# Optimization experiments

Measured on AMD Instinct MI355X. Metric: run time of the kernel, lower is better.

Reference implementation:

```python
import jax, jax.numpy as jnp
import numpy as np

N, K, D = 50000, 32, 128


def setup_inputs() -> dict:
    key = jax.random.key(0)
    k1, k2, k3, k4 = jax.random.split(key, 4)
    v_fea = jax.random.normal(k1, (N, D), dtype=jnp.float32)
    t_emb = jax.random.normal(k2, (N, D), dtype=jnp.float32)
    ef = jax.random.randint(k3, (N, K), 0, N, dtype=jnp.int64)
    # nn.Linear(2D, 2D, bias=False) weight, scaled like torch default init
    W = jax.random.normal(k4, (2 * D, 2 * D), dtype=jnp.float32) * (1.0 / np.sqrt(2 * D))
    return {"v_fea": v_fea, "t_emb": t_emb, "ef": ef, "W": W}


def reference(v_fea, t_emb, ef, W):
    # v: gathered neighbor features [N, K, D]
    v = v_fea[ef]
    # q: [N, 2D]; torch Linear applies x @ W.T
    q = jnp.concatenate([v_fea, t_emb], axis=-1)
    wq = q @ W.T                                   # [N, 2D]
    # k: [N, K, 2D]
    k = jnp.concatenate([v, t_emb[ef]], axis=-1)
    # per-edge score: bmm(k, wq[..., None]) -> [N, K]
    r = jnp.einsum("nkd,nd->nk", k, wq)
    r = jax.nn.softmax(r, axis=1)                  # softmax over neighbors
    # weighted sum over neighbors -> [N, D]
    ef_fea = jnp.einsum("nk,nkd->nd", r, v)
    return ef_fea
```

## Files before the change

kernel.cpp:

```cpp
#include <hip/hip_runtime.h>
#include <hip/hip_bf16.h>

#define D     128
#define TWO_D 256
#define KNB   32

typedef __attribute__((ext_vector_type(8))) short    s8;
typedef __attribute__((ext_vector_type(8))) _Float16 h8;
typedef __attribute__((ext_vector_type(2))) _Float16 h2v;
typedef __attribute__((ext_vector_type(4))) float    f4;

__device__ inline unsigned short f2h(float f) {
    return __builtin_bit_cast(unsigned short, (_Float16)f);
}
__device__ inline float h2f(unsigned short u) {
    return (float)__builtin_bit_cast(_Float16, u);
}

union v16u { s8 s; h2v h[4]; };

__device__ inline float dot8(s8 x, s8 w, float acc) {
#if __has_builtin(__builtin_amdgcn_fdot2)
    v16u ux, uw; ux.s = x; uw.s = w;
#pragma unroll
    for (int j = 0; j < 4; ++j)
        acc = __builtin_amdgcn_fdot2(ux.h[j], uw.h[j], acc, false);
#else
#pragma unroll
    for (int j = 0; j < 8; ++j)
        acc = fmaf(h2f((unsigned short)x[j]), h2f((unsigned short)w[j]), acc);
#endif
    return acc;
}

__global__ __launch_bounds__(256) void cast_kernel(
    const float* __restrict__ a, const float* __restrict__ b,
    unsigned short* __restrict__ oa, unsigned short* __restrict__ ob, int n4)
{
    int i = blockIdx.x * 256 + threadIdx.x;
    if (i >= n4) return;
    float4 x = ((const float4*)a)[i];
    float4 y = ((const float4*)b)[i];
    ushort4 px = make_ushort4(f2h(x.x), f2h(x.y), f2h(x.z), f2h(x.w));
    ushort4 py = make_ushort4(f2h(y.x), f2h(y.y), f2h(y.z), f2h(y.w));
    ((ushort4*)oa)[i] = px;
    ((ushort4*)ob)[i] = py;
}

#define BM 128
#define BN 128
#define BK 32
#define LDT 56

__global__ __launch_bounds__(256) void gemm_wq_mfma(
    const unsigned short* __restrict__ vh, const unsigned short* __restrict__ th,
    const float* __restrict__ W, unsigned short* __restrict__ wq_h, int M)
{
    __shared__ unsigned short As[BM][LDT];
    __shared__ unsigned short Bs[BN][LDT];

    const int tid  = threadIdx.x;
    const int w    = tid >> 6;
    const int lane = tid & 63;
    const int quad = lane >> 4;
    const int l16  = lane & 15;
    const int row0 = blockIdx.x * BM;
    const int i0   = blockIdx.y * BN;

    f4 acc[2][8] = {};

    const int srow = tid >> 1;
    const int seg  = tid & 1;
    int ga = row0 + srow; if (ga >= M) ga = M - 1;

    for (int kt = 0; kt < TWO_D; kt += BK) {
        const unsigned short* srcA = (kt < D) ? vh : th;
        const int kb = kt & (D - 1);
        const unsigned short* pa = srcA + (size_t)ga * D + kb + seg * 16;
        s8 a0 = *(const s8*)(pa);
        s8 a1 = *(const s8*)(pa + 8);
        const float* pb = W + (size_t)(i0 + srow) * TWO_D + kt + seg * 16;
        float4 b0 = *(const float4*)(pb);
        float4 b1 = *(const float4*)(pb + 4);
        float4 b2 = *(const float4*)(pb + 8);
        float4 b3 = *(const float4*)(pb + 12);

        __syncthreads();
        *(s8*)&As[srow][seg * 16]     = a0;
        *(s8*)&As[srow][seg * 16 + 8] = a1;
        {
            s8 q0, q1;
            q0[0]=(short)f2h(b0.x); q0[1]=(short)f2h(b0.y); q0[2]=(short)f2h(b0.z); q0[3]=(short)f2h(b0.w);
            q0[4]=(short)f2h(b1.x); q0[5]=(short)f2h(b1.y); q0[6]=(short)f2h(b1.z); q0[7]=(short)f2h(b1.w);
            q1[0]=(short)f2h(b2.x); q1[1]=(short)f2h(b2.y); q1[2]=(short)f2h(b2.z); q1[3]=(short)f2h(b2.w);
            q1[4]=(short)f2h(b3.x); q1[5]=(short)f2h(b3.y); q1[6]=(short)f2h(b3.z); q1[7]=(short)f2h(b3.w);
            *(s8*)&Bs[srow][seg * 16]     = q0;
            *(s8*)&Bs[srow][seg * 16 + 8] = q1;
        }
        __syncthreads();

        s8 af0 = *(const s8*)&As[w * 32 + l16][quad * 8];
        s8 af1 = *(const s8*)&As[w * 32 + 16 + l16][quad * 8];
#pragma unroll
        for (int nt = 0; nt < 8; ++nt) {
            s8 bf = *(const s8*)&Bs[nt * 16 + l16][quad * 8];
            acc[0][nt] = __builtin_amdgcn_mfma_f32_16x16x32_f16(
                __builtin_bit_cast(h8, af0), __builtin_bit_cast(h8, bf), acc[0][nt], 0, 0, 0);
            acc[1][nt] = __builtin_amdgcn_mfma_f32_16x16x32_f16(
                __builtin_bit_cast(h8, af1), __builtin_bit_cast(h8, bf), acc[1][nt], 0, 0, 0);
        }
    }

#pragma unroll
    for (int mt = 0; mt < 2; ++mt) {
#pragma unroll
        for (int nt = 0; nt < 8; ++nt) {
#pragma unroll
            for (int r = 0; r < 4; ++r) {
                int grow = row0 + w * 32 + mt * 16 + quad * 4 + r;
                if (grow < M)
                    wq_h[(size_t)grow * TWO_D + i0 + nt * 16 + l16] = f2h(acc[mt][nt][r]);
            }
        }
    }
}

__global__ __launch_bounds__(256) void attn_kernel(
    const unsigned short* __restrict__ vh, const unsigned short* __restrict__ th,
    const int* __restrict__ ef, const unsigned short* __restrict__ wq_h,
    float* __restrict__ outp, int M)
{
    __shared__ unsigned short v_cache[4][KNB][D];

    const int lane = threadIdx.x & 63;
    const int w    = threadIdx.x >> 6;
    const int n    = blockIdx.x * 4 + w;
    if (n >= M) return;

    const int l16  = lane & 15;
    const int gsel = (lane >> 4) & 1;
    const unsigned short* gsrc = (lane < 32) ? vh : th;

    s8 wq8 = *(const s8*)(wq_h + (size_t)n * TWO_D + ((lane >> 5) << 7) + l16 * 8);

    int eidx = 0;
    if (lane < KNB) eidx = ef[n * KNB + lane];

    s8 xs[16];
#pragma unroll
    for (int kk = 0; kk < 16; ++kk) {
        int e = __shfl(eidx, 2 * kk + gsel, 64);
        xs[kk] = *(const s8*)(gsrc + (size_t)e * D + l16 * 8);
    }

    float myscore = -1e30f;
#pragma unroll
    for (int kk = 0; kk < 16; ++kk) {
        const int k = 2 * kk;
        if (lane < 32) *(s8*)&v_cache[w][k + gsel][l16 * 8] = xs[kk];
        float p = dot8(xs[kk], wq8, 0.f);
#pragma unroll
        for (int off = 8; off > 0; off >>= 1) p += __shfl_xor(p, off, 64);
        p += __shfl_xor(p, 32, 64);
        float po = __shfl_xor(p, 16, 64);
        float s_even = gsel ? po : p;
        float s_odd  = gsel ? p  : po;
        if (lane == k)     myscore = s_even;
        if (lane == k + 1) myscore = s_odd;
    }

    float mx = myscore;
#pragma unroll
    for (int off = 16; off > 0; off >>= 1) mx = fmaxf(mx, __shfl_xor(mx, off, 64));
    float ex  = __expf(myscore - mx);
    float sum = ex;
#pragma unroll
    for (int off = 16; off > 0; off >>= 1) sum += __shfl_xor(sum, off, 64);
    float r = ex / sum;

    float2 o = make_float2(0.f, 0.f);
#pragma unroll
    for (int k = 0; k < KNB; ++k) {
        float rk = __shfl(r, k, 64);
        unsigned int pq = *(const unsigned int*)&v_cache[w][k][lane * 2];
        o.x = fmaf(rk, h2f((unsigned short)(pq & 0xFFFFu)), o.x);
        o.y = fmaf(rk, h2f((unsigned short)(pq >> 16)), o.y);
    }
    *(float2*)(outp + (size_t)n * D + lane * 2) = o;
}

extern "C" void kernel_launch(void* const* d_in, const int* in_sizes, int n_in,
                              void* d_out, int out_size, void* d_ws, size_t ws_size,
                              hipStream_t stream)
{
    const float* v_fea = (const float*)d_in[0];
    const float* t_emb = (const float*)d_in[1];
    const int*   ef    = (const int*)d_in[2];
    const float* W     = (const float*)d_in[3];
    float* outp = (float*)d_out;

    const int M = in_sizes[0] / D;
    char* ws = (char*)d_ws;
    unsigned short* wq_h = (unsigned short*)ws;
    unsigned short* vh   = (unsigned short*)(ws + (size_t)M * TWO_D * 2);
    unsigned short* th   = (unsigned short*)(ws + (size_t)M * TWO_D * 2 + (size_t)M * D * 2);

    const int n4 = M * D / 4;
    cast_kernel<<<(n4 + 255) / 256, 256, 0, stream>>>(v_fea, t_emb, vh, th, n4);

    dim3 gg((M + BM - 1) / BM, TWO_D / BN);
    gemm_wq_mfma<<<gg, 256, 0, stream>>>(vh, th, W, wq_h, M);
    attn_kernel<<<(M + 3) / 4, 256, 0, stream>>>(vh, th, ef, wq_h, outp, M);
}
```

Before: 230.0 us.

## Interleave fp16 v/t rows and use single-pass online-softmax gather attention

The cast kernel now writes v_fea and t_emb into one interleaved fp16 buffer of shape [N, 2D]. Each gathered neighbour therefore becomes a single contiguous 512-byte row, and the GEMM reads its A operand from that one buffer. The attention kernel drops the LDS cache. Each 16-lane group handles one neighbour per step, and the kernel uses an online (running-max) softmax with register accumulation, software-prefetching the second half of the neighbour rows. This is meant to cut the scattered gather transactions, the LDS traffic and the separate softmax passes. The cost is extra lane shuffles, wasted accumulation on the t half of each row, and higher register pressure.

```diff
diff --git a/kernel.cpp b/kernel.cpp
--- a/kernel.cpp
+++ b/kernel.cpp
@@ -35,16 +35,22 @@
 
 __global__ __launch_bounds__(256) void cast_kernel(
     const float* __restrict__ a, const float* __restrict__ b,
-    unsigned short* __restrict__ oa, unsigned short* __restrict__ ob, int n4)
+    unsigned short* __restrict__ ph, int total)
 {
     int i = blockIdx.x * 256 + threadIdx.x;
-    if (i >= n4) return;
-    float4 x = ((const float4*)a)[i];
-    float4 y = ((const float4*)b)[i];
-    ushort4 px = make_ushort4(f2h(x.x), f2h(x.y), f2h(x.z), f2h(x.w));
-    ushort4 py = make_ushort4(f2h(y.x), f2h(y.y), f2h(y.z), f2h(y.w));
-    ((ushort4*)oa)[i] = px;
-    ((ushort4*)ob)[i] = py;
+    if (i >= total) return;
+    int n = i >> 4, j = i & 15;
+    const float4* pv = (const float4*)(a + (size_t)n * D + j * 8);
+    const float4* pt = (const float4*)(b + (size_t)n * D + j * 8);
+    float4 v0 = pv[0], v1 = pv[1];
+    float4 t0 = pt[0], t1 = pt[1];
+    s8 qv, qt;
+    qv[0]=(short)f2h(v0.x); qv[1]=(short)f2h(v0.y); qv[2]=(short)f2h(v0.z); qv[3]=(short)f2h(v0.w);
+    qv[4]=(short)f2h(v1.x); qv[5]=(short)f2h(v1.y); qv[6]=(short)f2h(v1.z); qv[7]=(short)f2h(v1.w);
+    qt[0]=(short)f2h(t0.x); qt[1]=(short)f2h(t0.y); qt[2]=(short)f2h(t0.z); qt[3]=(short)f2h(t0.w);
+    qt[4]=(short)f2h(t1.x); qt[5]=(short)f2h(t1.y); qt[6]=(short)f2h(t1.z); qt[7]=(short)f2h(t1.w);
+    *(s8*)(ph + (size_t)n * TWO_D + j * 8)     = qv;
+    *(s8*)(ph + (size_t)n * TWO_D + D + j * 8) = qt;
 }
 
 #define BM 128
@@ -53,7 +59,7 @@
 #define LDT 56
 
 __global__ __launch_bounds__(256) void gemm_wq_mfma(
-    const unsigned short* __restrict__ vh, const unsigned short* __restrict__ th,
+    const unsigned short* __restrict__ ph,
     const float* __restrict__ W, unsigned short* __restrict__ wq_h, int M)
 {
     __shared__ unsigned short As[BM][LDT];
@@ -74,9 +80,7 @@
     int ga = row0 + srow; if (ga >= M) ga = M - 1;
 
     for (int kt = 0; kt < TWO_D; kt += BK) {
-        const unsigned short* srcA = (kt < D) ? vh : th;
-        const int kb = kt & (D - 1);
-        const unsigned short* pa = srcA + (size_t)ga * D + kb + seg * 16;
+        const unsigned short* pa = ph + (size_t)ga * TWO_D + kt + seg * 16;
         s8 a0 = *(const s8*)(pa);
         s8 a1 = *(const s8*)(pa + 8);
         const float* pb = W + (size_t)(i0 + srow) * TWO_D + kt + seg * 16;
@@ -126,67 +130,90 @@
 }
 
 __global__ __launch_bounds__(256) void attn_kernel(
-    const unsigned short* __restrict__ vh, const unsigned short* __restrict__ th,
-    const int* __restrict__ ef, const unsigned short* __restrict__ wq_h,
-    float* __restrict__ outp, int M)
-{
-    __shared__ unsigned short v_cache[4][KNB][D];
-
+    const unsigned short* __restrict__ ph, const int* __restrict__ ef,
+    const unsigned short* __restrict__ wq_h, float* __restrict__ outp, int M)
+{
     const int lane = threadIdx.x & 63;
     const int w    = threadIdx.x >> 6;
     const int n    = blockIdx.x * 4 + w;
     if (n >= M) return;
 
-    const int l16  = lane & 15;
-    const int gsel = (lane >> 4) & 1;
-    const unsigned short* gsrc = (lane < 32) ? vh : th;
-
-    s8 wq8 = *(const s8*)(wq_h + (size_t)n * TWO_D + ((lane >> 5) << 7) + l16 * 8);
+    const int g = lane >> 4;
+    const int j = lane & 15;
+
+    const unsigned short* wp = wq_h + (size_t)n * TWO_D + j * 16;
+    s8 wqa = *(const s8*)(wp);
+    s8 wqb = *(const s8*)(wp + 8);
 
     int eidx = 0;
     if (lane < KNB) eidx = ef[n * KNB + lane];
 
-    s8 xs[16];
-#pragma unroll
-    for (int kk = 0; kk < 16; ++kk) {
-        int e = __shfl(eidx, 2 * kk + gsel, 64);
-        xs[kk] = *(const s8*)(gsrc + (size_t)e * D + l16 * 8);
-    }
-
-    float myscore = -1e30f;
-#pragma unroll
-    for (int kk = 0; kk < 16; ++kk) {
-        const int k = 2 * kk;
-        if (lane < 32) *(s8*)&v_cache[w][k + gsel][l16 * 8] = xs[kk];
-        float p = dot8(xs[kk], wq8, 0.f);
-#pragma unroll
-        for (int off = 8; off > 0; off >>= 1) p += __shfl_xor(p, off, 64);
-        p += __shfl_xor(p, 32, 64);
-        float po = __shfl_xor(p, 16, 64);
-        float s_even = gsel ? po : p;
-        float s_odd  = gsel ? p  : po;
-        if (lane == k)     myscore = s_even;
-        if (lane == k + 1) myscore = s_odd;
-    }
-
-    float mx = myscore;
-#pragma unroll
-    for (int off = 16; off > 0; off >>= 1) mx = fmaxf(mx, __shfl_xor(mx, off, 64));
-    float ex  = __expf(myscore - mx);
-    float sum = ex;
-#pragma unroll
-    for (int off = 16; off > 0; off >>= 1) sum += __shfl_xor(sum, off, 64);
-    float r = ex / sum;
-
-    float2 o = make_float2(0.f, 0.f);
-#pragma unroll
-    for (int k = 0; k < KNB; ++k) {
-        float rk = __shfl(r, k, 64);
-        unsigned int pq = *(const unsigned int*)&v_cache[w][k][lane * 2];
-        o.x = fmaf(rk, h2f((unsigned short)(pq & 0xFFFFu)), o.x);
-        o.y = fmaf(rk, h2f((unsigned short)(pq >> 16)), o.y);
-    }
-    *(float2*)(outp + (size_t)n * D + lane * 2) = o;
+    s8 xa[8], xb[8];
+#pragma unroll
+    for (int p = 0; p < 4; ++p) {
+        int e = __shfl(eidx, 4 * p + g, 64);
+        const unsigned short* rp = ph + (size_t)e * TWO_D + j * 16;
+        xa[p] = *(const s8*)(rp);
+        xb[p] = *(const s8*)(rp + 8);
+    }
+
+    float m = -1e30f, ssum = 0.f;
+    float o[16] = {};
+
+#pragma unroll
+    for (int p = 0; p < 8; ++p) {
+        if (p < 4) {
+            int e = __shfl(eidx, 4 * (p + 4) + g, 64);
+            const unsigned short* rp = ph + (size_t)e * TWO_D + j * 16;
+            xa[p + 4] = *(const s8*)(rp);
+            xb[p + 4] = *(const s8*)(rp + 8);
+        }
+        float s = dot8(xa[p], wqa, 0.f);
+        s = dot8(xb[p], wqb, s);
+#pragma unroll
+        for (int off = 8; off; off >>= 1) s += __shfl_xor(s, off, 64);
+        float sb = __shfl_xor(s, 16, 64);
+        float sc = __shfl_xor(s, 32, 64);
+        float sd = __shfl_xor(sb, 32, 64);
+        float mt = fmaxf(fmaxf(s, sb), fmaxf(sc, sd));
+        if (mt > m) {
+            float scale = __expf(m - mt);
+            ssum *= scale;
+#pragma unroll
+            for (int t = 0; t < 16; ++t) o[t] *= scale;
+            m = mt;
+        }
+        float e0 = __expf(s - m);
+        float e1 = __expf(sb - m);
+        float e2 = __expf(sc - m);
+        float e3 = __expf(sd - m);
+        ssum += (e0 + e1) + (e2 + e3);
+        v16u ua, ub; ua.s = xa[p]; ub.s = xb[p];
+#pragma unroll
+        for (int t = 0; t < 4; ++t) {
+            o[2*t]     = fmaf(e0, (float)ua.h[t][0], o[2*t]);
+            o[2*t+1]   = fmaf(e0, (float)ua.h[t][1], o[2*t+1]);
+            o[8+2*t]   = fmaf(e0, (float)ub.h[t][0], o[8+2*t]);
+            o[8+2*t+1] = fmaf(e0, (float)ub.h[t][1], o[8+2*t+1]);
+        }
+    }
+
+#pragma unroll
+    for (int t = 0; t < 16; ++t) {
+        o[t] += __shfl_xor(o[t], 16, 64);
+        o[t] += __shfl_xor(o[t], 32, 64);
+    }
+
+    if (lane < 8) {
+        float inv = 1.0f / ssum;
+        float* orow = outp + (size_t)n * D + lane * 16;
+#pragma unroll
+        for (int c = 0; c < 4; ++c) {
+            float4 st = make_float4(o[4*c] * inv, o[4*c+1] * inv,
+                                    o[4*c+2] * inv, o[4*c+3] * inv);
+            *(float4*)(orow + 4 * c) = st;
+        }
+    }
 }
 
 extern "C" void kernel_launch(void* const* d_in, const int* in_sizes, int n_in,
@@ -202,13 +229,12 @@
     const int M = in_sizes[0] / D;
     char* ws = (char*)d_ws;
     unsigned short* wq_h = (unsigned short*)ws;
-    unsigned short* vh   = (unsigned short*)(ws + (size_t)M * TWO_D * 2);
-    unsigned short* th   = (unsigned short*)(ws + (size_t)M * TWO_D * 2 + (size_t)M * D * 2);
-
-    const int n4 = M * D / 4;
-    cast_kernel<<<(n4 + 255) / 256, 256, 0, stream>>>(v_fea, t_emb, vh, th, n4);
+    unsigned short* ph   = (unsigned short*)(ws + (size_t)M * TWO_D * 2);
+
+    const int total = M * 16;
+    cast_kernel<<<(total + 255) / 256, 256, 0, stream>>>(v_fea, t_emb, ph, total);
 
     dim3 gg((M + BM - 1) / BM, TWO_D / BN);
-    gemm_wq_mfma<<<gg, 256, 0, stream>>>(vh, th, W, wq_h, M);
-    attn_kernel<<<(M + 3) / 4, 256, 0, stream>>>(vh, th, ef, wq_h, outp, M);
-}
+    gemm_wq_mfma<<<gg, 256, 0, stream>>>(ph, W, wq_h, M);
+    attn_kernel<<<(M + 3) / 4, 256, 0, stream>>>(ph, ef, wq_h, outp, M);
+}
```

New measurement: 225.6 us. No clear change (-1.9%).
